# Kernel optimization log

Measured on AMD Instinct MI355X. Metric: run time of the kernel, lower is better.

Reference implementation:

```python
import jax, jax.numpy as jnp
import numpy as np

NEG_INF = -1e9  # same masked_fill constant as the torch module
ALPHA = 0.1     # LeakyReLU negative slope


def setup_inputs() -> dict:
    key = jax.random.key(0)
    k1, k2, k3, k4, k5 = jax.random.split(key, 5)
    B, N, Din, Dout = 8, 2048, 512, 512
    features = jax.random.normal(k1, (B, N, Din), dtype=jnp.float32)
    graph = jax.random.randint(k2, (B, N, N), 0, 2, dtype=jnp.int64)
    # xavier_uniform with gain=1.414: limit = gain*sqrt(6/(fan_in+fan_out))
    lim_w = 1.414 * np.sqrt(6.0 / (Din + Dout))
    w = jax.random.uniform(k3, (Din, Dout), jnp.float32, -lim_w, lim_w)
    lim_a = 1.414 * np.sqrt(6.0 / (Dout + 1))
    a1 = jax.random.uniform(k4, (Dout, 1), jnp.float32, -lim_a, lim_a)
    a2 = jax.random.uniform(k5, (Dout, 1), jnp.float32, -lim_a, lim_a)
    return {"features": features, "graph": graph, "w": w, "a1": a1, "a2": a2}


def reference(features, graph, w, a1, a2):
    # hidden: [B, N, Dout]
    hidden = jnp.einsum("bni,io->bno", features, w)
    s1 = hidden @ a1  # [B, N, 1] -> broadcasts over columns
    s2 = hidden @ a2  # [B, N, 1] -> transposed broadcasts over rows
    # e[b,i,j] = leaky_relu(s1[b,i] + s2[b,j])
    e = jax.nn.leaky_relu(s1 + jnp.swapaxes(s2, 1, 2), negative_slope=ALPHA)
    e = jnp.where(graph == 0, NEG_INF, e)
    attn = jax.nn.softmax(e, axis=-1)  # [B, N, N]; dropout p=0 -> identity
    h_prime = jnp.einsum("bij,bjo->bio", attn, hidden)
    return jax.nn.elu(h_prime)  # concat=True
```

## Files before the change

### kernel.cpp

```cpp
#include <hip/hip_runtime.h>
#include <math.h>

#define B_ 8
#define N_ 2048
#define D_ 512
#define NROWS (B_ * N_)
#define NEG_ALPHA 0.1f

typedef __bf16 bf16;
typedef __bf16 bf16x4 __attribute__((ext_vector_type(4)));
typedef __bf16 bf16x8 __attribute__((ext_vector_type(8)));
typedef float f32x4 __attribute__((ext_vector_type(4)));
typedef float f32x16 __attribute__((ext_vector_type(16)));

#define HTB_BATCH ((D_ / 32) * (N_ / 16) * 512)

__global__ __launch_bounds__(256) void k_pre0(const float* __restrict__ W,
                                              bf16* __restrict__ Wt,
                                              const float* __restrict__ a1,
                                              const float* __restrict__ a2,
                                              float* __restrict__ wa1,
                                              float* __restrict__ wa2) {
  __shared__ float tile[64][65];
  const int bid = blockIdx.x;
  if (bid < 64) {
    const int din0 = (bid >> 3) * 64, dout0 = (bid & 7) * 64;
    const int tx = threadIdx.x & 63, tg = threadIdx.x >> 6;
#pragma unroll
    for (int rr = 0; rr < 16; ++rr) {
      int dr = tg * 16 + rr;
      tile[dr][tx] = W[(size_t)(din0 + dr) * D_ + dout0 + tx];
    }
    __syncthreads();
#pragma unroll
    for (int rr = 0; rr < 4; ++rr) {
      int dl = rr * 16 + (threadIdx.x >> 4);
      int nl = (threadIdx.x & 15) * 4;
      bf16x4 v = {(bf16)tile[nl][dl], (bf16)tile[nl + 1][dl],
                  (bf16)tile[nl + 2][dl], (bf16)tile[nl + 3][dl]};
      *(bf16x4*)&Wt[(size_t)(dout0 + dl) * D_ + din0 + nl] = v;
    }
  } else {
    const int wv = threadIdx.x >> 6, lane = threadIdx.x & 63;
    const int row = (bid - 64) * 4 + wv;
    const float* wr = W + (size_t)row * D_;
    float d1 = 0.f, d2 = 0.f;
#pragma unroll
    for (int p = 0; p < 8; ++p) {
      int c = lane + p * 64;
      float w = wr[c];
      d1 = fmaf(w, a1[c], d1);
      d2 = fmaf(w, a2[c], d2);
    }
#pragma unroll
    for (int off = 32; off > 0; off >>= 1) {
      d1 += __shfl_down(d1, off, 64);
      d2 += __shfl_down(d2, off, 64);
    }
    if (lane == 0) {
      wa1[row] = d1;
      wa2[row] = d2;
    }
  }
}

__global__ __launch_bounds__(256) void k_scores_x(const float* __restrict__ X,
                                                  const float* __restrict__ wa1,
                                                  const float* __restrict__ wa2,
                                                  float* __restrict__ s1,
                                                  float* __restrict__ s2,
                                                  const int* __restrict__ G,
                                                  unsigned int* __restrict__ GB) {
  const int wv = threadIdx.x >> 6, lane = threadIdx.x & 63;
  const int r = blockIdx.x * 4 + wv;
  const float* x = X + (size_t)r * D_;
  float d1 = 0.f, d2 = 0.f;
#pragma unroll
  for (int p = 0; p < 2; ++p) {
    int c = lane * 4 + p * 256;
    float4 xv = *(const float4*)&x[c];
    float4 w1 = *(const float4*)&wa1[c];
    float4 w2 = *(const float4*)&wa2[c];
    d1 += xv.x * w1.x + xv.y * w1.y + xv.z * w1.z + xv.w * w1.w;
    d2 += xv.x * w2.x + xv.y * w2.y + xv.z * w2.z + xv.w * w2.w;
  }
  {
    const size_t g = (size_t)blockIdx.x * 256 + threadIdx.x;
    const int* src = G + g * 32;
    unsigned int bits = 0;
#pragma unroll
    for (int p = 0; p < 8; ++p) {
      int4 v = *(const int4*)&src[p * 4];
      bits |= (unsigned)(v.x != 0) << (p * 4);
      bits |= (unsigned)(v.y != 0) << (p * 4 + 1);
      bits |= (unsigned)(v.z != 0) << (p * 4 + 2);
      bits |= (unsigned)(v.w != 0) << (p * 4 + 3);
    }
    GB[g] = bits;
  }
#pragma unroll
  for (int off = 32; off > 0; off >>= 1) {
    d1 += __shfl_down(d1, off, 64);
    d2 += __shfl_down(d2, off, 64);
  }
  if (lane == 0) {
    s1[r] = d1;
    s2[r] = d2;
  }
}

#define LDH 40

__global__ __launch_bounds__(256, 2) void k_hiddenT(const float* __restrict__ X,
                                                    const bf16* __restrict__ Wt,
                                                    bf16* __restrict__ HtB) {
  __shared__ bf16 As[128][LDH];
  __shared__ bf16 Bs[128][LDH];
  const int t = threadIdx.x;
  const int m0 = blockIdx.y * 128;
  const int n0 = blockIdx.x * 128;
  const int lane = t & 63, w = t >> 6;
  const int wm = w >> 1, wn = w & 1;
  const int l15 = lane & 15, q = lane >> 4;

  f32x4 acc[4][4];
#pragma unroll
  for (int i = 0; i < 4; ++i)
#pragma unroll
    for (int j = 0; j < 4; ++j) acc[i][j] = (f32x4){0.f, 0.f, 0.f, 0.f};

  bf16x8 av[2];
  float4 bv[4];
#pragma unroll
  for (int p = 0; p < 2; ++p) {
    int s = t + p * 256;
    av[p] = *(const bf16x8*)&Wt[(size_t)(m0 + (s >> 2)) * D_ + (s & 3) * 8];
  }
#pragma unroll
  for (int p = 0; p < 4; ++p) {
    int s = t + p * 256;
    bv[p] = *(const float4*)&X[(size_t)(n0 + (s >> 3)) * D_ + (s & 7) * 4];
  }

  for (int k0 = 0; k0 < D_; k0 += 32) {
    __syncthreads();
#pragma unroll
    for (int p = 0; p < 2; ++p) {
      int s = t + p * 256;
      *(bf16x8*)&As[s >> 2][(s & 3) * 8] = av[p];
    }
#pragma unroll
    for (int p = 0; p < 4; ++p) {
      int s = t + p * 256;
      float4 v = bv[p];
      bf16x4 h = {(bf16)v.x, (bf16)v.y, (bf16)v.z, (bf16)v.w};
      *(bf16x4*)&Bs[s >> 3][(s & 7) * 4] = h;
    }
    __syncthreads();
    if (k0 + 32 < D_) {
#pragma unroll
      for (int p = 0; p < 2; ++p) {
        int s = t + p * 256;
        av[p] = *(const bf16x8*)&Wt[(size_t)(m0 + (s >> 2)) * D_ + k0 + 32 + (s & 3) * 8];
      }
#pragma unroll
      for (int p = 0; p < 4; ++p) {
        int s = t + p * 256;
        bv[p] = *(const float4*)&X[(size_t)(n0 + (s >> 3)) * D_ + k0 + 32 + (s & 7) * 4];
      }
    }
    bf16x8 a[4], bb[4];
#pragma unroll
    for (int i = 0; i < 4; ++i)
      a[i] = *(const bf16x8*)&As[wm * 64 + i * 16 + l15][q * 8];
#pragma unroll
    for (int j = 0; j < 4; ++j)
      bb[j] = *(const bf16x8*)&Bs[wn * 64 + j * 16 + l15][q * 8];
#pragma unroll
    for (int i = 0; i < 4; ++i)
#pragma unroll
      for (int j = 0; j < 4; ++j)
        acc[i][j] =
            __builtin_amdgcn_mfma_f32_16x16x32_bf16(a[i], bb[j], acc[i][j], 0, 0, 0);
  }
#pragma unroll
  for (int i = 0; i < 4; ++i)
#pragma unroll
    for (int r = 0; r < 4; ++r) {
      int dout = m0 + wm * 64 + i * 16 + q * 4 + r;
#pragma unroll
      for (int j = 0; j < 4; ++j) {
        int row = n0 + wn * 64 + j * 16 + l15;
        int bb_ = row >> 11;
        int jj = row & (N_ - 1);
        size_t addr = (size_t)bb_ * HTB_BATCH +
                      ((size_t)((dout >> 5) * (N_ / 16) + (jj >> 4)) * 64 +
                       ((jj >> 3) & 1) * 32 + (dout & 31)) *
                          8 +
                      (jj & 7);
        HtB[addr] = (bf16)acc[i][j][r];
      }
    }
}

#define AT_BM 64
#define AT_BK 32
#define LDP 40
#define NIT (N_ / AT_BK)
#define GROW 272

__global__ __launch_bounds__(512, 4) void k_attn(const bf16* __restrict__ HtB,
                                                 const unsigned char* __restrict__ GB,
                                                 const float* __restrict__ s1,
                                                 const float* __restrict__ s2,
                                                 float* __restrict__ out) {
  __shared__ __align__(16) bf16 Ps[2][AT_BM][LDP];
  __shared__ __align__(16) bf16 Hs[2][8192];
  __shared__ float s2s[N_];
  __shared__ __align__(16) unsigned char gb_s[AT_BM][GROW];
  __shared__ float sum_part[AT_BM][8];
  __shared__ float row_sum[AT_BM];

  const int t = threadIdx.x;
  const int bid = blockIdx.x;
  const int b = bid & 7;
  const int i0 = ((bid >> 3) & 31) * AT_BM;
  const int ds = bid >> 8;
  const int lane = t & 63, w = t >> 6;
  const int r31 = lane & 31, hf = lane >> 5;
  const int dch = ds * 8 + w;

  const bf16* Hb = HtB + (size_t)b * HTB_BATCH;
  const unsigned char* GBb = GB + ((size_t)b * N_ + i0) * (N_ / 8);

  for (int c = t; c < N_; c += 512) s2s[c] = s2[b * N_ + c];
  {
    int gr = t >> 3, gc = (t & 7) * 32;
    int4 w0 = *(const int4*)&GBb[(size_t)gr * (N_ / 8) + gc];
    int4 w1 = *(const int4*)&GBb[(size_t)gr * (N_ / 8) + gc + 16];
    *(int4*)&gb_s[gr][gc] = w0;
    *(int4*)&gb_s[gr][gc + 16] = w1;
  }

  const int pi = t >> 3;
  const int c8 = t & 7;
  const int pj = c8 * 4;
  const float s1r = s1[b * N_ + i0 + pi];
  float rsum = 0.f;

  f32x16 acc[2];
#pragma unroll
  for (int i = 0; i < 2; ++i)
#pragma unroll
    for (int r = 0; r < 16; ++r) acc[i][r] = 0.f;

  bf16* HsF = &Hs[0][0];
#pragma unroll
  for (int jo = 0; jo < 2; ++jo) {
    const bf16* src = &Hb[((size_t)dch * (N_ / 16) + jo) * 512 + lane * 8];
    __builtin_amdgcn_global_load_lds(
        (const __attribute__((address_space(1))) void*)src,
        (__attribute__((address_space(3))) void*)&HsF[w * 1024 + jo * 512], 16,
        0, 0);
  }

  __syncthreads();

#pragma unroll 1
  for (int it = 0; it < NIT; ++it) {
    const int cur = it & 1;
    {
      unsigned gbits = (unsigned)(gb_s[pi][it * 4 + (c8 >> 1)]) >> ((c8 & 1) * 4);
      f32x4 sv = *(const f32x4*)&s2s[it * AT_BK + pj];
      float pv[4];
#pragma unroll
      for (int q_ = 0; q_ < 4; ++q_) {
        float e = s1r + sv[q_];
        e = (e > 0.f) ? e : NEG_ALPHA * e;
        pv[q_] = ((gbits >> q_) & 1) ? __expf(e) : 0.f;
        rsum += pv[q_];
      }
      bf16x4 pb = {(bf16)pv[0], (bf16)pv[1], (bf16)pv[2], (bf16)pv[3]};
      *(bf16x4*)&Ps[cur][pi][pj] = pb;
    }
    {
      const int jn = (it + 1 < NIT) ? it + 1 : 0;
#pragma unroll
      for (int jo = 0; jo < 2; ++jo) {
        const bf16* src =
            &Hb[((size_t)dch * (N_ / 16) + jn * 2 + jo) * 512 + lane * 8];
        __builtin_amdgcn_global_load_lds(
            (const __attribute__((address_space(1))) void*)src,
            (__attribute__((address_space(3))) void*)
                &HsF[(cur ^ 1) * 8192 + w * 1024 + jo * 512],
            16, 0, 0);
      }
    }
    asm volatile("s_waitcnt lgkmcnt(0)" ::: "memory");
    __builtin_amdgcn_sched_barrier(0);
    __builtin_amdgcn_s_barrier();
    __builtin_amdgcn_sched_barrier(0);
    asm volatile("s_waitcnt vmcnt(2)" ::: "memory");
    __builtin_amdgcn_sched_barrier(0);
#pragma unroll
    for (int ks = 0; ks < 2; ++ks) {
      const int ko = ks * 16 + hf * 8;
      bf16x8 a0 = *(const bf16x8*)&Ps[cur][r31][ko];
      bf16x8 a1 = *(const bf16x8*)&Ps[cur][32 + r31][ko];
      bf16x8 bB = *(const bf16x8*)&HsF[cur * 8192 + w * 1024 + ks * 512 + lane * 8];
      acc[0] = __builtin_amdgcn_mfma_f32_32x32x16_bf16(a0, bB, acc[0], 0, 0, 0);
      acc[1] = __builtin_amdgcn_mfma_f32_32x32x16_bf16(a1, bB, acc[1], 0, 0, 0);
    }
  }

  sum_part[pi][c8] = rsum;
  __syncthreads();
  if (t < AT_BM) {
    float s = 0.f;
#pragma unroll
    for (int k = 0; k < 8; ++k) s += sum_part[t][k];
    row_sum[t] = s;
  }
  __syncthreads();

#pragma unroll
  for (int mt = 0; mt < 2; ++mt) {
    float inv[16];
#pragma unroll
    for (int r = 0; r < 16; ++r)
      inv[r] = 1.f / row_sum[mt * 32 + (r & 3) + 8 * (r >> 2) + 4 * hf];
    const int d = ds * 256 + w * 32 + r31;
#pragma unroll
    for (int r = 0; r < 16; ++r) {
      int i = mt * 32 + (r & 3) + 8 * (r >> 2) + 4 * hf;
      float x = acc[mt][r] * inv[r];
      out[((size_t)b * N_ + i0 + i) * D_ + d] = (x > 0.f) ? x : (__expf(x) - 1.f);
    }
  }
}

extern "C" void kernel_launch(void* const* d_in, const int* in_sizes, int n_in,
                              void* d_out, int out_size, void* d_ws,
                              size_t ws_size, hipStream_t stream) {
  const float* X = (const float*)d_in[0];
  const int* graph = (const int*)d_in[1];
  const float* W = (const float*)d_in[2];
  const float* a1 = (const float*)d_in[3];
  const float* a2 = (const float*)d_in[4];
  float* out = (float*)d_out;

  char* ws = (char*)d_ws;
  bf16* Wt = (bf16*)ws;
  bf16* HtB = (bf16*)(ws + (1 << 19));
  unsigned int* GBw = (unsigned int*)(ws + (1 << 19) + (16 << 20));
  float* s1 = (float*)(ws + (1 << 19) + (21 << 20));
  float* s2 = s1 + NROWS;
  float* wa1 = s2 + NROWS;
  float* wa2 = wa1 + D_;

  hipLaunchKernelGGL(k_pre0, dim3(192), dim3(256), 0, stream, W, Wt, a1, a2,
                     wa1, wa2);
  hipLaunchKernelGGL(k_scores_x, dim3(NROWS / 4), dim3(256), 0, stream, X, wa1,
                     wa2, s1, s2, graph, GBw);
  hipLaunchKernelGGL(k_hiddenT, dim3(NROWS / 128, D_ / 128), dim3(256), 0,
                     stream, X, Wt, HtB);
  hipLaunchKernelGGL(k_attn, dim3(N_ / AT_BM * B_ * 2), dim3(512), 0, stream,
                     HtB, (const unsigned char*)GBw, s1, s2, out);
}
```

Before: 303.0 us.

## Read int graph directly in attention kernel, pre-convert X to bf16

Drops the separate pass that packed the int32 adjacency matrix into bitmasks. The attention kernel now streams graph int4 values straight from global memory, prefetched two iterations ahead in registers, and the loop is unrolled by two with s_setprio raised around the MFMA block. The scores kernel also writes a bf16 copy of X, so the hidden GEMM loads half the bytes and skips in-loop conversion. The trade-off is that k_attn is split into two blocks per batch/row tile (ds = bid>>8), so each block now reads the full 4-byte-per-element graph rows itself, doubling int32 graph traffic compared with a single compact read plus bitmask reuse.

New measurement: 277.3 us. 1.09x faster.

```diff
diff --git a/kernel.cpp b/kernel.cpp
--- a/kernel.cpp
+++ b/kernel.cpp
@@ -69,8 +69,7 @@
                                                   const float* __restrict__ wa2,
                                                   float* __restrict__ s1,
                                                   float* __restrict__ s2,
-                                                  const int* __restrict__ G,
-                                                  unsigned int* __restrict__ GB) {
+                                                  bf16* __restrict__ Xb) {
   const int wv = threadIdx.x >> 6, lane = threadIdx.x & 63;
   const int r = blockIdx.x * 4 + wv;
   const float* x = X + (size_t)r * D_;
@@ -83,20 +82,8 @@
     float4 w2 = *(const float4*)&wa2[c];
     d1 += xv.x * w1.x + xv.y * w1.y + xv.z * w1.z + xv.w * w1.w;
     d2 += xv.x * w2.x + xv.y * w2.y + xv.z * w2.z + xv.w * w2.w;
-  }
-  {
-    const size_t g = (size_t)blockIdx.x * 256 + threadIdx.x;
-    const int* src = G + g * 32;
-    unsigned int bits = 0;
-#pragma unroll
-    for (int p = 0; p < 8; ++p) {
-      int4 v = *(const int4*)&src[p * 4];
-      bits |= (unsigned)(v.x != 0) << (p * 4);
-      bits |= (unsigned)(v.y != 0) << (p * 4 + 1);
-      bits |= (unsigned)(v.z != 0) << (p * 4 + 2);
-      bits |= (unsigned)(v.w != 0) << (p * 4 + 3);
-    }
-    GB[g] = bits;
+    bf16x4 h = {(bf16)xv.x, (bf16)xv.y, (bf16)xv.z, (bf16)xv.w};
+    *(bf16x4*)&Xb[(size_t)r * D_ + c] = h;
   }
 #pragma unroll
   for (int off = 32; off > 0; off >>= 1) {
@@ -111,7 +98,7 @@
 
 #define LDH 40
 
-__global__ __launch_bounds__(256, 2) void k_hiddenT(const float* __restrict__ X,
+__global__ __launch_bounds__(256, 2) void k_hiddenT(const bf16* __restrict__ Xb,
                                                     const bf16* __restrict__ Wt,
                                                     bf16* __restrict__ HtB) {
   __shared__ bf16 As[128][LDH];
@@ -129,17 +116,12 @@
 #pragma unroll
     for (int j = 0; j < 4; ++j) acc[i][j] = (f32x4){0.f, 0.f, 0.f, 0.f};
 
-  bf16x8 av[2];
-  float4 bv[4];
+  bf16x8 av[2], bv[2];
 #pragma unroll
   for (int p = 0; p < 2; ++p) {
     int s = t + p * 256;
     av[p] = *(const bf16x8*)&Wt[(size_t)(m0 + (s >> 2)) * D_ + (s & 3) * 8];
-  }
-#pragma unroll
-  for (int p = 0; p < 4; ++p) {
-    int s = t + p * 256;
-    bv[p] = *(const float4*)&X[(size_t)(n0 + (s >> 3)) * D_ + (s & 7) * 4];
+    bv[p] = *(const bf16x8*)&Xb[(size_t)(n0 + (s >> 2)) * D_ + (s & 3) * 8];
   }
 
   for (int k0 = 0; k0 < D_; k0 += 32) {
@@ -148,13 +130,7 @@
     for (int p = 0; p < 2; ++p) {
       int s = t + p * 256;
       *(bf16x8*)&As[s >> 2][(s & 3) * 8] = av[p];
-    }
-#pragma unroll
-    for (int p = 0; p < 4; ++p) {
-      int s = t + p * 256;
-      float4 v = bv[p];
-      bf16x4 h = {(bf16)v.x, (bf16)v.y, (bf16)v.z, (bf16)v.w};
-      *(bf16x4*)&Bs[s >> 3][(s & 7) * 4] = h;
+      *(bf16x8*)&Bs[s >> 2][(s & 3) * 8] = bv[p];
     }
     __syncthreads();
     if (k0 + 32 < D_) {
@@ -162,11 +138,7 @@
       for (int p = 0; p < 2; ++p) {
         int s = t + p * 256;
         av[p] = *(const bf16x8*)&Wt[(size_t)(m0 + (s >> 2)) * D_ + k0 + 32 + (s & 3) * 8];
-      }
-#pragma unroll
-      for (int p = 0; p < 4; ++p) {
-        int s = t + p * 256;
-        bv[p] = *(const float4*)&X[(size_t)(n0 + (s >> 3)) * D_ + k0 + 32 + (s & 7) * 4];
+        bv[p] = *(const bf16x8*)&Xb[(size_t)(n0 + (s >> 2)) * D_ + k0 + 32 + (s & 3) * 8];
       }
     }
     bf16x8 a[4], bb[4];
@@ -207,17 +179,68 @@
 #define AT_BK 32
 #define LDP 40
 #define NIT (N_ / AT_BK)
-#define GROW 272
+
+#define ATTN_IT(IT, GCUR)                                                      \
+  {                                                                            \
+    const int it_ = (IT);                                                      \
+    const int cur_ = it_ & 1;                                                  \
+                     \
+    int itn_ = it_ + 2;                                                        \
+    int jg_ = (itn_ < NIT) ? itn_ * AT_BK : 0;                                 \
+    int4 gnew_ = *(const int4*)&Gb[(size_t)pi * N_ + jg_ + pj];                \
+    {                               \
+      f32x4 sv = *(const f32x4*)&s2s[it_ * AT_BK + pj];                        \
+      int gg[4] = {GCUR.x, GCUR.y, GCUR.z, GCUR.w};                            \
+      float pv[4];                                                             \
+      _Pragma("unroll") for (int q_ = 0; q_ < 4; ++q_) {                       \
+        float e = s1r + sv[q_];                                                \
+        e = (e > 0.f) ? e : NEG_ALPHA * e;                                     \
+        pv[q_] = (gg[q_] != 0) ? __expf(e) : 0.f;                              \
+        rsum += pv[q_];                                                        \
+      }                                                                        \
+      bf16x4 pb = {(bf16)pv[0], (bf16)pv[1], (bf16)pv[2], (bf16)pv[3]};        \
+      *(bf16x4*)&Ps[cur_][pi][pj] = pb;                                        \
+    }                                                                          \
+    {                      \
+      const int jn_ = (it_ + 1 < NIT) ? it_ + 1 : 0;                           \
+      _Pragma("unroll") for (int jo = 0; jo < 2; ++jo) {                       \
+        const bf16* src =                                                      \
+            &Hb[((size_t)dch * (N_ / 16) + jn_ * 2 + jo) * 512 + lane * 8];    \
+        __builtin_amdgcn_global_load_lds(                                      \
+            (const __attribute__((address_space(1))) void*)src,                \
+            (__attribute__((address_space(3))) void*)                          \
+                &HsF[(cur_ ^ 1) * 8192 + w * 1024 + jo * 512],                 \
+            16, 0, 0);                                                         \
+      }                                                                        \
+    }                                                                          \
+    asm volatile("s_waitcnt lgkmcnt(0)" ::: "memory");                         \
+    __builtin_amdgcn_sched_barrier(0);                                         \
+    __builtin_amdgcn_s_barrier();                                              \
+    __builtin_amdgcn_sched_barrier(0);                                         \
+    asm volatile("s_waitcnt vmcnt(3)" ::: "memory");                           \
+    __builtin_amdgcn_sched_barrier(0);                                         \
+    __builtin_amdgcn_s_setprio(1);                                             \
+    _Pragma("unroll") for (int ks = 0; ks < 2; ++ks) {                         \
+      const int ko = ks * 16 + hf * 8;                                         \
+      bf16x8 a0 = *(const bf16x8*)&Ps[cur_][r31][ko];                          \
+      bf16x8 a1 = *(const bf16x8*)&Ps[cur_][32 + r31][ko];                     \
+      bf16x8 bB =                                                              \
+          *(const bf16x8*)&HsF[cur_ * 8192 + w * 1024 + ks * 512 + lane * 8];  \
+      acc[0] = __builtin_amdgcn_mfma_f32_32x32x16_bf16(a0, bB, acc[0], 0, 0, 0); \
+      acc[1] = __builtin_amdgcn_mfma_f32_32x32x16_bf16(a1, bB, acc[1], 0, 0, 0); \
+    }                                                                          \
+    __builtin_amdgcn_s_setprio(0);                                             \
+    GCUR = gnew_;                                                              \
+  }
 
 __global__ __launch_bounds__(512, 4) void k_attn(const bf16* __restrict__ HtB,
-                                                 const unsigned char* __restrict__ GB,
+                                                 const int* __restrict__ graph,
                                                  const float* __restrict__ s1,
                                                  const float* __restrict__ s2,
                                                  float* __restrict__ out) {
   __shared__ __align__(16) bf16 Ps[2][AT_BM][LDP];
   __shared__ __align__(16) bf16 Hs[2][8192];
   __shared__ float s2s[N_];
-  __shared__ __align__(16) unsigned char gb_s[AT_BM][GROW];
   __shared__ float sum_part[AT_BM][8];
   __shared__ float row_sum[AT_BM];
 
@@ -231,16 +254,9 @@
   const int dch = ds * 8 + w;
 
   const bf16* Hb = HtB + (size_t)b * HTB_BATCH;
-  const unsigned char* GBb = GB + ((size_t)b * N_ + i0) * (N_ / 8);
+  const int* Gb = graph + ((size_t)b * N_ + i0) * N_;
 
   for (int c = t; c < N_; c += 512) s2s[c] = s2[b * N_ + c];
-  {
-    int gr = t >> 3, gc = (t & 7) * 32;
-    int4 w0 = *(const int4*)&GBb[(size_t)gr * (N_ / 8) + gc];
-    int4 w1 = *(const int4*)&GBb[(size_t)gr * (N_ / 8) + gc + 16];
-    *(int4*)&gb_s[gr][gc] = w0;
-    *(int4*)&gb_s[gr][gc + 16] = w1;
-  }
 
   const int pi = t >> 3;
   const int c8 = t & 7;
@@ -254,6 +270,8 @@
 #pragma unroll
     for (int r = 0; r < 16; ++r) acc[i][r] = 0.f;
 
+  int4 gA = *(const int4*)&Gb[(size_t)pi * N_ + pj];
+  int4 gB = *(const int4*)&Gb[(size_t)pi * N_ + AT_BK + pj];
   bf16* HsF = &Hs[0][0];
 #pragma unroll
   for (int jo = 0; jo < 2; ++jo) {
@@ -267,50 +285,9 @@
   __syncthreads();
 
 #pragma unroll 1
-  for (int it = 0; it < NIT; ++it) {
-    const int cur = it & 1;
-    {
-      unsigned gbits = (unsigned)(gb_s[pi][it * 4 + (c8 >> 1)]) >> ((c8 & 1) * 4);
-      f32x4 sv = *(const f32x4*)&s2s[it * AT_BK + pj];
-      float pv[4];
-#pragma unroll
-      for (int q_ = 0; q_ < 4; ++q_) {
-        float e = s1r + sv[q_];
-        e = (e > 0.f) ? e : NEG_ALPHA * e;
-        pv[q_] = ((gbits >> q_) & 1) ? __expf(e) : 0.f;
-        rsum += pv[q_];
-      }
-      bf16x4 pb = {(bf16)pv[0], (bf16)pv[1], (bf16)pv[2], (bf16)pv[3]};
-      *(bf16x4*)&Ps[cur][pi][pj] = pb;
-    }
-    {
-      const int jn = (it + 1 < NIT) ? it + 1 : 0;
-#pragma unroll
-      for (int jo = 0; jo < 2; ++jo) {
-        const bf16* src =
-            &Hb[((size_t)dch * (N_ / 16) + jn * 2 + jo) * 512 + lane * 8];
-        __builtin_amdgcn_global_load_lds(
-            (const __attribute__((address_space(1))) void*)src,
-            (__attribute__((address_space(3))) void*)
-                &HsF[(cur ^ 1) * 8192 + w * 1024 + jo * 512],
-            16, 0, 0);
-      }
-    }
-    asm volatile("s_waitcnt lgkmcnt(0)" ::: "memory");
-    __builtin_amdgcn_sched_barrier(0);
-    __builtin_amdgcn_s_barrier();
-    __builtin_amdgcn_sched_barrier(0);
-    asm volatile("s_waitcnt vmcnt(2)" ::: "memory");
-    __builtin_amdgcn_sched_barrier(0);
-#pragma unroll
-    for (int ks = 0; ks < 2; ++ks) {
-      const int ko = ks * 16 + hf * 8;
-      bf16x8 a0 = *(const bf16x8*)&Ps[cur][r31][ko];
-      bf16x8 a1 = *(const bf16x8*)&Ps[cur][32 + r31][ko];
-      bf16x8 bB = *(const bf16x8*)&HsF[cur * 8192 + w * 1024 + ks * 512 + lane * 8];
-      acc[0] = __builtin_amdgcn_mfma_f32_32x32x16_bf16(a0, bB, acc[0], 0, 0, 0);
-      acc[1] = __builtin_amdgcn_mfma_f32_32x32x16_bf16(a1, bB, acc[1], 0, 0, 0);
-    }
+  for (int i2 = 0; i2 < NIT / 2; ++i2) {
+    ATTN_IT(i2 * 2, gA);
+    ATTN_IT(i2 * 2 + 1, gB);
   }
 
   sum_part[pi][c8] = rsum;
@@ -352,8 +329,8 @@
   char* ws = (char*)d_ws;
   bf16* Wt = (bf16*)ws;
   bf16* HtB = (bf16*)(ws + (1 << 19));
-  unsigned int* GBw = (unsigned int*)(ws + (1 << 19) + (16 << 20));
-  float* s1 = (float*)(ws + (1 << 19) + (21 << 20));
+  bf16* Xb = (bf16*)(ws + (1 << 19) + (16 << 20));
+  float* s1 = (float*)(ws + (1 << 19) + (32 << 20));
   float* s2 = s1 + NROWS;
   float* wa1 = s2 + NROWS;
   float* wa2 = wa1 + D_;
@@ -361,9 +338,9 @@
   hipLaunchKernelGGL(k_pre0, dim3(192), dim3(256), 0, stream, W, Wt, a1, a2,
                      wa1, wa2);
   hipLaunchKernelGGL(k_scores_x, dim3(NROWS / 4), dim3(256), 0, stream, X, wa1,
-                     wa2, s1, s2, graph, GBw);
+                     wa2, s1, s2, Xb);
   hipLaunchKernelGGL(k_hiddenT, dim3(NROWS / 128, D_ / 128), dim3(256), 0,
-                     stream, X, Wt, HtB);
+                     stream, Xb, Wt, HtB);
   hipLaunchKernelGGL(k_attn, dim3(N_ / AT_BM * B_ * 2), dim3(512), 0, stream,
-                     HtB, (const unsigned char*)GBw, s1, s2, out);
-}
+                     HtB, graph, s1, s2, out);
+}
```
